# Kernel tuning notes

Hardware: AMD Instinct MI355X
Metric: run time of the kernel (lower is better)

## Reference

```python
import jax, jax.numpy as jnp
from jax import lax
import numpy as np

B, T = 32, 64
E = 64        # embed_dim
U = 32        # num_measurements
D0, D1 = 300, 100
S = 9         # speaker_num
CELL = 64     # output_cell_dim
C = 6         # n_classes
EPS = 1e-12


def setup_inputs() -> dict:
    key = jax.random.key(0)
    ks = jax.random.split(key, 16)
    sc = 1.0 / np.sqrt(E)
    n = lambda i, shape, s=1.0: (jax.random.normal(ks[i], shape, jnp.float32) * s)
    return {
        "x0": n(0, (B, T, D0)),
        "x1": n(1, (B, T, D1)),
        "smask": jax.random.uniform(ks[2], (B, T, S), jnp.float32),
        "umask": jnp.ones((B, T), jnp.float32),
        "W_ih0": n(3, (4 * E, D0), sc), "W_hh0": n(4, (4 * E, E), sc),
        "b_ih0": n(5, (4 * E,), sc), "b_hh0": n(6, (4 * E,), sc),
        "W_ih1": n(7, (4 * E, D1), sc), "W_hh1": n(8, (4 * E, E), sc),
        "b_ih1": n(9, (4 * E,), sc), "b_hh1": n(10, (4 * E,), sc),
        "phase_table": jax.random.uniform(ks[11], (S, E), jnp.float32, -np.pi, np.pi),
        "meas_kernel": jax.random.uniform(ks[12], (U, E, 2), jnp.float32),
        "W1": n(13, (CELL, 2 * U), 0.1), "b1": jnp.zeros((CELL,), jnp.float32),
        "W2": n(14, (C, CELL), 0.1), "b2": jnp.zeros((C,), jnp.float32),
    }


def _lstm_tanh(x, um, Wih, Whh, bih, bhh):
    # torch.nn.LSTMCell (gate order i,f,g,o) + extra tanh applied to h each step;
    # the tanh-ed h is carried as the recurrent state (dropout = identity in eval).
    b, t, _ = x.shape
    e = Whh.shape[1]

    def step(carry, inp):
        h, c = carry
        xt, ut = inp
        g = (xt * ut[:, None]) @ Wih.T + bih + h @ Whh.T + bhh
        i, f, gg, o = jnp.split(g, 4, axis=-1)
        c = jax.nn.sigmoid(f) * c + jax.nn.sigmoid(i) * jnp.tanh(gg)
        h = jnp.tanh(jax.nn.sigmoid(o) * jnp.tanh(c))
        return (h, c), h

    h0 = jnp.zeros((b, e), x.dtype)
    _, hs = lax.scan(step, (h0, h0), (jnp.swapaxes(x, 0, 1), um.T))
    return jnp.swapaxes(hs, 0, 1)  # (B,T,E)


def _measure(amp, phase, kernel):
    # pure state v = cos(phase)*amp + i sin(phase)*amp; rho = |v><v|
    r = jnp.cos(phase) * amp
    im = jnp.sin(phase) * amp
    rho_r = jnp.einsum('bti,btj->btij', r, r) + jnp.einsum('bti,btj->btij', im, im)
    rho_i = jnp.einsum('bti,btj->btij', im, r) - jnp.einsum('bti,btj->btij', r, im)
    u = kernel.shape[0]
    norm = jnp.clip(jnp.linalg.norm(kernel.reshape(u, -1), axis=-1), EPS)
    kn = kernel / norm[:, None, None]
    kr, ki = kn[..., 0], kn[..., 1]
    Pr = jnp.einsum('ui,uj->uij', kr, kr) + jnp.einsum('ui,uj->uij', ki, ki)
    Pi = jnp.einsum('ui,uj->uij', ki, kr) - jnp.einsum('ui,uj->uij', kr, ki)
    return jnp.einsum('btij,uij->btu', rho_r, Pr) - jnp.einsum('btij,uij->btu', rho_i, Pi)


def reference(x0, x1, smask, umask, W_ih0, W_hh0, b_ih0, b_hh0,
              W_ih1, W_hh1, b_ih1, b_hh1, phase_table, meas_kernel,
              W1, b1, W2, b2):
    h0 = _lstm_tanh(x0, umask, W_ih0, W_hh0, b_ih0, b_hh0)
    h1 = _lstm_tanh(x1, umask, W_ih1, W_hh1, b_ih1, b_hh1)
    norm = lambda h: h / jnp.clip(jnp.linalg.norm(h, axis=-1, keepdims=True), EPS)
    phase = phase_table[jnp.argmax(smask, axis=-1)]  # (B,T,E); table shared by both modalities
    m = jnp.concatenate([_measure(norm(h0), phase, meas_kernel),
                         _measure(norm(h1), phase, meas_kernel)], axis=-1)
    hid = jax.nn.relu(m @ W1.T + b1)
    pred = jnp.tanh(hid @ W2.T + b2)
    return jax.nn.log_softmax(pred, axis=2)
```

## Files before the change

kernel.cpp:

```cpp
#include <hip/hip_runtime.h>

typedef unsigned short ushort_t;
typedef unsigned int uint_t;
typedef float f32x2 __attribute__((ext_vector_type(2)));

__device__ __forceinline__ float bf2f(ushort_t v) {
  union { uint_t u; float f; } x; x.u = ((uint_t)v) << 16; return x.f;
}
__device__ __forceinline__ float lo16(uint_t u) {
  union { uint_t u; float f; } x; x.u = u << 16; return x.f;
}
__device__ __forceinline__ float hi16(uint_t u) {
  union { uint_t u; float f; } x; x.u = u & 0xffff0000u; return x.f;
}
__device__ __forceinline__ ushort_t f2bf(float f) {
  union { float f; uint_t u; } x; x.f = f;
  uint_t u = x.u;
  uint_t r = (u + 0x7fffu + ((u >> 16) & 1u)) >> 16;
  return (ushort_t)r;
}
__device__ __forceinline__ bool is_bf16(const void* um) {
  return *(const uint_t*)um == 0x3F803F80u;
}
__device__ __forceinline__ float ld_dual(const void* p, int i, bool isb) {
  return isb ? bf2f(((const ushort_t*)p)[i]) : ((const float*)p)[i];
}
__device__ __forceinline__ float frcp(float x) { return __builtin_amdgcn_rcpf(x); }
__device__ __forceinline__ float fsig(float x) { return frcp(1.f + __expf(-x)); }
__device__ __forceinline__ float ftanh(float x) {
  return fmaf(2.f, frcp(1.f + __expf(-2.f * x)), -1.f);
}

#if defined(__has_builtin)
#if __has_builtin(__builtin_elementwise_fma)
#define FMA2(a, b, c) __builtin_elementwise_fma((a), (b), (c))
#endif
#endif
#ifndef FMA2
__device__ __forceinline__ f32x2 fma2_fb(f32x2 a, f32x2 b, f32x2 c) {
  c.x = fmaf(a.x, b.x, c.x); c.y = fmaf(a.y, b.y, c.y); return c;
}
#define FMA2(a, b, c) fma2_fb((a), (b), (c))
#endif

__device__ __forceinline__ float dpp_add_xor1(float v) {
  const int r = __builtin_amdgcn_update_dpp(0, __float_as_int(v), 0xB1, 0xF, 0xF, true);
  return v + __int_as_float(r);
}
__device__ __forceinline__ float dpp_add_xor2(float v) {
  const int r = __builtin_amdgcn_update_dpp(0, __float_as_int(v), 0x4E, 0xF, 0xF, true);
  return v + __int_as_float(r);
}

#define PROJ_LDW 108

template <int D, bool ISB>
__device__ __forceinline__ void proj_body(
    const void* __restrict__ x, const void* __restrict__ um,
    const void* __restrict__ Wih, const void* __restrict__ bih,
    const void* __restrict__ bhh, float* __restrict__ xw,
    int rtile, int gtile, float* __restrict__ xs, float* __restrict__ ws)
{
  const int tid = threadIdx.x;
  const int r0 = rtile * 32;
  const int g0 = gtile * 32;
  const int rt = tid >> 4;
  const int gt = tid & 15;
  float a00 = 0.f, a01 = 0.f, a10 = 0.f, a11 = 0.f;

  for (int kt = 0; kt < D; kt += 100) {
    for (int i = tid; i < 800; i += 256) {
      const int r = i / 25;
      const int k4 = (i - r * 25) * 4;
      if (ISB) {
        const uint2 xv = *(const uint2*)((const ushort_t*)x + (r0 + r) * D + kt + k4);
        *(float4*)(xs + r * PROJ_LDW + k4) =
            make_float4(lo16(xv.x), hi16(xv.x), lo16(xv.y), hi16(xv.y));
        const uint2 wv = *(const uint2*)((const ushort_t*)Wih + (g0 + r) * D + kt + k4);
        *(float4*)(ws + r * PROJ_LDW + k4) =
            make_float4(lo16(wv.x), hi16(wv.x), lo16(wv.y), hi16(wv.y));
      } else {
        *(float4*)(xs + r * PROJ_LDW + k4) =
            *(const float4*)((const float*)x + (r0 + r) * D + kt + k4);
        *(float4*)(ws + r * PROJ_LDW + k4) =
            *(const float4*)((const float*)Wih + (g0 + r) * D + kt + k4);
      }
    }
    __syncthreads();
#pragma unroll 5
    for (int k = 0; k < 100; k += 4) {
      const float4 xa = *(const float4*)(xs + rt * PROJ_LDW + k);
      const float4 xb = *(const float4*)(xs + (rt + 16) * PROJ_LDW + k);
      const float4 wa = *(const float4*)(ws + gt * PROJ_LDW + k);
      const float4 wb = *(const float4*)(ws + (gt + 16) * PROJ_LDW + k);
      a00 = fmaf(xa.x, wa.x, a00); a00 = fmaf(xa.y, wa.y, a00);
      a00 = fmaf(xa.z, wa.z, a00); a00 = fmaf(xa.w, wa.w, a00);
      a01 = fmaf(xa.x, wb.x, a01); a01 = fmaf(xa.y, wb.y, a01);
      a01 = fmaf(xa.z, wb.z, a01); a01 = fmaf(xa.w, wb.w, a01);
      a10 = fmaf(xb.x, wa.x, a10); a10 = fmaf(xb.y, wa.y, a10);
      a10 = fmaf(xb.z, wa.z, a10); a10 = fmaf(xb.w, wa.w, a10);
      a11 = fmaf(xb.x, wb.x, a11); a11 = fmaf(xb.y, wb.y, a11);
      a11 = fmaf(xb.z, wb.z, a11); a11 = fmaf(xb.w, wb.w, a11);
    }
    __syncthreads();
  }

  const int ra = r0 + rt, rb = ra + 16;
  const int ga = g0 + gt, gb = ga + 16;
  const float ba = ld_dual(bih, ga, ISB) + ld_dual(bhh, ga, ISB);
  const float bb = ld_dual(bih, gb, ISB) + ld_dual(bhh, gb, ISB);
  const float ua = ld_dual(um, ra, ISB);
  const float ub = ld_dual(um, rb, ISB);
  const int pa = ((ga & 63) << 2) | (ga >> 6);
  const int pb = ((gb & 63) << 2) | (gb >> 6);
  xw[ra * 256 + pa] = fmaf(a00, ua, ba);
  xw[ra * 256 + pb] = fmaf(a01, ua, bb);
  xw[rb * 256 + pa] = fmaf(a10, ub, ba);
  xw[rb * 256 + pb] = fmaf(a11, ub, bb);
}

__global__ __launch_bounds__(256) void proj_both(
    const void* __restrict__ x0, const void* __restrict__ x1,
    const void* __restrict__ um,
    const void* __restrict__ Wih0, const void* __restrict__ bih0,
    const void* __restrict__ bhh0,
    const void* __restrict__ Wih1, const void* __restrict__ bih1,
    const void* __restrict__ bhh1,
    float* __restrict__ xw0, float* __restrict__ xw1)
{
  __shared__ __align__(16) float xs[32 * PROJ_LDW];
  __shared__ __align__(16) float ws[32 * PROJ_LDW];
  const bool isb = is_bf16(um);
  const int bid = blockIdx.x;
  const int l = bid >> 9;
  const int t = bid & 511;
  const int rtile = t >> 3;
  const int gtile = t & 7;
  if (l == 0) {
    if (isb) proj_body<300, true>(x0, um, Wih0, bih0, bhh0, xw0, rtile, gtile, xs, ws);
    else     proj_body<300, false>(x0, um, Wih0, bih0, bhh0, xw0, rtile, gtile, xs, ws);
  } else {
    if (isb) proj_body<100, true>(x1, um, Wih1, bih1, bhh1, xw1, rtile, gtile, xs, ws);
    else     proj_body<100, false>(x1, um, Wih1, bih1, bhh1, xw1, rtile, gtile, xs, ws);
  }
}

__global__ __launch_bounds__(256, 1) void lstm_k(
    const float* __restrict__ xw0, const float* __restrict__ xw1,
    const void* __restrict__ Whh0, const void* __restrict__ Whh1,
    const void* __restrict__ um,
    float* __restrict__ h0r, float* __restrict__ h1r)
{
  __shared__ __align__(16) float xws[64 * 256];
  __shared__ __align__(16) float hist[65 * 64];

  const int bid = blockIdx.x;
  const int l = bid >> 5;
  const int b = bid & 31;
  const float* xw = (l ? xw1 : xw0) + b * 64 * 256;
  const void* Whh = (l ? Whh1 : Whh0);
  float* hr = (l ? h1r : h0r) + b * 64 * 64;
  const int tid = threadIdx.x;
  const int e = tid >> 2;
  const int q = tid & 3;
  const int k0 = q << 4;
  const bool isb = is_bf16(um);

  for (int i = tid; i < 4096; i += 256)
    *(float4*)(xws + i * 4) = *(const float4*)(xw + i * 4);
  if (tid < 64) hist[tid] = 0.f;

  f32x2 w2[4][8];
  if (isb) {
#pragma unroll
    for (int t = 0; t < 4; ++t) {
      const ushort_t* wr = (const ushort_t*)Whh + (t * 64 + e) * 64 + k0;
#pragma unroll
      for (int j = 0; j < 16; j += 8) {
        const uint4 v = *(const uint4*)(wr + j);
        w2[t][(j >> 1) + 0] = f32x2{lo16(v.x), hi16(v.x)};
        w2[t][(j >> 1) + 1] = f32x2{lo16(v.y), hi16(v.y)};
        w2[t][(j >> 1) + 2] = f32x2{lo16(v.z), hi16(v.z)};
        w2[t][(j >> 1) + 3] = f32x2{lo16(v.w), hi16(v.w)};
      }
    }
  } else {
#pragma unroll
    for (int t = 0; t < 4; ++t) {
      const float* wr = (const float*)Whh + (t * 64 + e) * 64 + k0;
#pragma unroll
      for (int j = 0; j < 16; j += 4) {
        const float4 v = *(const float4*)(wr + j);
        w2[t][(j >> 1) + 0] = f32x2{v.x, v.y};
        w2[t][(j >> 1) + 1] = f32x2{v.z, v.w};
      }
    }
  }
  __syncthreads();

  float c = 0.f;
  float gin = xws[tid];
  for (int s = 0; s < 64; ++s) {
    const float* hp = hist + s * 64 + k0;
    f32x2 P0 = {q == 0 ? gin : 0.f, 0.f};
    f32x2 P1 = {q == 1 ? gin : 0.f, 0.f};
    f32x2 P2 = {q == 2 ? gin : 0.f, 0.f};
    f32x2 P3 = {q == 3 ? gin : 0.f, 0.f};
#pragma unroll
    for (int j = 0; j < 16; j += 4) {
      const float4 hv = *(const float4*)(hp + j);
      const f32x2 hA = {hv.x, hv.y}, hB = {hv.z, hv.w};
      const int jp = j >> 1;
      P0 = FMA2(w2[0][jp], hA, P0); P0 = FMA2(w2[0][jp + 1], hB, P0);
      P1 = FMA2(w2[1][jp], hA, P1); P1 = FMA2(w2[1][jp + 1], hB, P1);
      P2 = FMA2(w2[2][jp], hA, P2); P2 = FMA2(w2[2][jp + 1], hB, P2);
      P3 = FMA2(w2[3][jp], hA, P3); P3 = FMA2(w2[3][jp + 1], hB, P3);
    }
    float p0 = P0.x + P0.y;
    float p1 = P1.x + P1.y;
    float p2 = P2.x + P2.y;
    float p3 = P3.x + P3.y;
    p0 = dpp_add_xor1(p0); p0 = dpp_add_xor2(p0);
    p1 = dpp_add_xor1(p1); p1 = dpp_add_xor2(p1);
    p2 = dpp_add_xor1(p2); p2 = dpp_add_xor2(p2);
    p3 = dpp_add_xor1(p3); p3 = dpp_add_xor2(p3);
    const float yi = fsig(p0);
    const float yf = fsig(p1);
    const float yg = ftanh(p2);
    const float yo = fsig(p3);
    c = fmaf(yf, c, yi * yg);
    const float h = ftanh(yo * ftanh(c));
    if (q == 0) hist[(s + 1) * 64 + e] = h;
    if (s + 1 < 64) gin = xws[(s + 1) * 256 + tid];
    __syncthreads();
  }
  for (int i = tid; i < 1024; i += 256)
    *(float4*)(hr + i * 4) = *(const float4*)(hist + 64 + i * 4);
}

__global__ __launch_bounds__(256) void head_k(
    const float* __restrict__ h0r, const float* __restrict__ h1r,
    const void* __restrict__ smask, const void* __restrict__ um,
    const void* __restrict__ ptab, const void* __restrict__ mker,
    const void* __restrict__ W1, const void* __restrict__ b1,
    const void* __restrict__ W2, const void* __restrict__ b2,
    void* __restrict__ out)
{
  __shared__ float2 knT[64][32];
  __shared__ float w1T[64][65];
  __shared__ float w2T[64][9];
  __shared__ float b1s[64];
  __shared__ float b2s[8];
  __shared__ float rim[4][4][64];
  __shared__ float msh[4][64];
  __shared__ float hidsh[4][64];
  __shared__ float psh[4][8];

  const int tid = threadIdx.x;
  const bool isb = is_bf16(um);
  {
    const int u = tid >> 3, sub = tid & 7;
    float vr[8], vi[8];
    float ssq = 0.f;
#pragma unroll
    for (int qq = 0; qq < 8; ++qq) {
      const int e = sub * 8 + qq;
      if (isb) {
        const uint_t kk = ((const uint_t*)mker)[u * 64 + e];
        vr[qq] = lo16(kk); vi[qq] = hi16(kk);
      } else {
        const float2 kk = ((const float2*)mker)[u * 64 + e];
        vr[qq] = kk.x; vi[qq] = kk.y;
      }
      ssq = fmaf(vr[qq], vr[qq], ssq);
      ssq = fmaf(vi[qq], vi[qq], ssq);
    }
    ssq += __shfl_xor(ssq, 1);
    ssq += __shfl_xor(ssq, 2);
    ssq += __shfl_xor(ssq, 4);
    const float rn = 1.f / fmaxf(sqrtf(ssq), 1e-12f);
#pragma unroll
    for (int qq = 0; qq < 8; ++qq) {
      const int e = sub * 8 + qq;
      knT[e][u] = make_float2(vr[qq] * rn, vi[qq] * rn);
    }
  }
  for (int i = tid; i < 4096; i += 256) {
    const int j = i >> 6, ll = i & 63;
    w1T[ll][j] = ld_dual(W1, i, isb);
  }
  if (tid < 64) b1s[tid] = ld_dual(b1, tid, isb);
  for (int i = tid; i < 384; i += 256) {
    const int cc = i >> 6, j = i & 63;
    w2T[j][cc] = ld_dual(W2, i, isb);
  }
  if (tid < 6) b2s[tid] = ld_dual(b2, tid, isb);
  __syncthreads();

  const int wv = tid >> 6, lane = tid & 63;
  const int item = blockIdx.x * 4 + wv;
  const float h0raw = h0r[item * 64 + lane];
  const float h1raw = h1r[item * 64 + lane];
  float ss0 = h0raw * h0raw, ss1 = h1raw * h1raw;
#pragma unroll
  for (int m = 1; m < 64; m <<= 1) {
    ss0 += __shfl_xor(ss0, m);
    ss1 += __shfl_xor(ss1, m);
  }
  const float h0 = h0raw / fmaxf(sqrtf(ss0), 1e-12f);
  const float h1 = h1raw / fmaxf(sqrtf(ss1), 1e-12f);

  int idx = 0;
  if (lane == 0) {
    float best = -1e30f;
#pragma unroll
    for (int si = 0; si < 9; ++si) {
      const float v = ld_dual(smask, item * 9 + si, isb);
      if (v > best) { best = v; idx = si; }
    }
  }
  idx = __shfl(idx, 0, 64);
  const float ph = ld_dual(ptab, idx * 64 + lane, isb);
  float sr, cr;
  __sincosf(ph, &sr, &cr);
  rim[wv][0][lane] = cr * h0;
  rim[wv][1][lane] = sr * h0;
  rim[wv][2][lane] = cr * h1;
  rim[wv][3][lane] = sr * h1;
  __syncthreads();
  {
    const int u = lane & 31;
    const float* ra = rim[wv][(lane >= 32) ? 2 : 0];
    const float* ia = rim[wv][(lane >= 32) ? 3 : 1];
    float ar = 0.f, ai = 0.f;
#pragma unroll 8
    for (int e = 0; e < 64; ++e) {
      const float2 k = knT[e][u];
      const float rr = ra[e], ii = ia[e];
      ar = fmaf(rr, k.x, ar);
      ar = fmaf(-ii, k.y, ar);
      ai = fmaf(rr, k.y, ai);
      ai = fmaf(ii, k.x, ai);
    }
    msh[wv][lane] = fmaf(ar, ar, ai * ai);
  }
  __syncthreads();
  {
    float acc = b1s[lane];
#pragma unroll 8
    for (int L = 0; L < 64; ++L)
      acc = fmaf(msh[wv][L], w1T[L][lane], acc);
    hidsh[wv][lane] = fmaxf(acc, 0.f);
  }
  __syncthreads();
  if (lane < 6) {
    float a2 = b2s[lane];
#pragma unroll 8
    for (int j = 0; j < 64; ++j)
      a2 = fmaf(hidsh[wv][j], w2T[j][lane], a2);
    psh[wv][lane] = ftanh(a2);
  }
  __syncthreads();
  if (lane < 6) {
    const float p = psh[wv][lane];
    float mx = psh[wv][0];
#pragma unroll
    for (int cc = 1; cc < 6; ++cc) mx = fmaxf(mx, psh[wv][cc]);
    float sum = 0.f;
#pragma unroll
    for (int cc = 0; cc < 6; ++cc) sum += __expf(psh[wv][cc] - mx);
    const float res = p - mx - __logf(sum);
    if (isb) ((ushort_t*)out)[item * 6 + lane] = f2bf(res);
    else     ((float*)out)[item * 6 + lane] = res;
  }
}

extern "C" void kernel_launch(void* const* d_in, const int* in_sizes, int n_in,
                              void* d_out, int out_size, void* d_ws, size_t ws_size,
                              hipStream_t stream)
{
  (void)in_sizes; (void)n_in; (void)out_size; (void)ws_size;
  const void* x0    = d_in[0];
  const void* x1    = d_in[1];
  const void* smask = d_in[2];
  const void* um    = d_in[3];
  const void* Wih0  = d_in[4];
  const void* Whh0  = d_in[5];
  const void* bih0  = d_in[6];
  const void* bhh0  = d_in[7];
  const void* Wih1  = d_in[8];
  const void* Whh1  = d_in[9];
  const void* bih1  = d_in[10];
  const void* bhh1  = d_in[11];
  const void* ptab  = d_in[12];
  const void* mker  = d_in[13];
  const void* W1    = d_in[14];
  const void* b1    = d_in[15];
  const void* W2    = d_in[16];
  const void* b2    = d_in[17];

  float* xw0 = (float*)d_ws;
  float* xw1 = xw0 + 2048 * 256;
  float* h0r = xw1 + 2048 * 256;
  float* h1r = h0r + 2048 * 64;

  hipLaunchKernelGGL(proj_both, dim3(1024), dim3(256), 0, stream,
                     x0, x1, um, Wih0, bih0, bhh0, Wih1, bih1, bhh1,
                     xw0, xw1);
  hipLaunchKernelGGL(lstm_k, dim3(64), dim3(256), 0, stream,
                     xw0, xw1, Whh0, Whh1, um, h0r, h1r);
  hipLaunchKernelGGL(head_k, dim3(512), dim3(256), 0, stream,
                     h0r, h1r, smask, um, ptab, mker, W1, b1, W2, b2,
                     d_out);
}
```

Baseline: 148.4 us.

## Map each LSTM sequence to one wavefront to remove block barriers

Each batch sequence of the recurrent kernel now runs on a single 64-lane wavefront, with four sequences per block and 16 blocks in total. Each lane holds a full 64-wide row for all four gates in registers, so the DPP cross-lane reductions and the per-step __syncthreads disappear. The hidden state moves through a small per-wave LDS buffer. Input projections are prefetched from global memory one step ahead, and h is written straight to global memory each step. In exchange, each lane runs four times more serial FMAs per step, needs about 256 registers just for the weights, and the grid shrinks to 16 blocks.

```diff
diff --git a/kernel.cpp b/kernel.cpp
--- a/kernel.cpp
+++ b/kernel.cpp
@@ -42,15 +42,6 @@
 }
 #define FMA2(a, b, c) fma2_fb((a), (b), (c))
 #endif
-
-__device__ __forceinline__ float dpp_add_xor1(float v) {
-  const int r = __builtin_amdgcn_update_dpp(0, __float_as_int(v), 0xB1, 0xF, 0xF, true);
-  return v + __int_as_float(r);
-}
-__device__ __forceinline__ float dpp_add_xor2(float v) {
-  const int r = __builtin_amdgcn_update_dpp(0, __float_as_int(v), 0x4E, 0xF, 0xF, true);
-  return v + __int_as_float(r);
-}
 
 #define PROJ_LDW 108
 
@@ -151,64 +142,57 @@
     const void* __restrict__ um,
     float* __restrict__ h0r, float* __restrict__ h1r)
 {
-  __shared__ __align__(16) float xws[64 * 256];
-  __shared__ __align__(16) float hist[65 * 64];
-
+  __shared__ __align__(16) float wstage[256 * 68];
+  __shared__ __align__(16) float hsh[4][64];
+
+  const int tid = threadIdx.x;
+  const int wv = tid >> 6, lane = tid & 63;
   const int bid = blockIdx.x;
-  const int l = bid >> 5;
-  const int b = bid & 31;
+  const int l = bid >> 3;
+  const int b = (bid & 7) * 4 + wv;
   const float* xw = (l ? xw1 : xw0) + b * 64 * 256;
   const void* Whh = (l ? Whh1 : Whh0);
   float* hr = (l ? h1r : h0r) + b * 64 * 64;
-  const int tid = threadIdx.x;
-  const int e = tid >> 2;
-  const int q = tid & 3;
-  const int k0 = q << 4;
   const bool isb = is_bf16(um);
 
-  for (int i = tid; i < 4096; i += 256)
-    *(float4*)(xws + i * 4) = *(const float4*)(xw + i * 4);
-  if (tid < 64) hist[tid] = 0.f;
-
-  f32x2 w2[4][8];
-  if (isb) {
-#pragma unroll
-    for (int t = 0; t < 4; ++t) {
-      const ushort_t* wr = (const ushort_t*)Whh + (t * 64 + e) * 64 + k0;
-#pragma unroll
-      for (int j = 0; j < 16; j += 8) {
-        const uint4 v = *(const uint4*)(wr + j);
-        w2[t][(j >> 1) + 0] = f32x2{lo16(v.x), hi16(v.x)};
-        w2[t][(j >> 1) + 1] = f32x2{lo16(v.y), hi16(v.y)};
-        w2[t][(j >> 1) + 2] = f32x2{lo16(v.z), hi16(v.z)};
-        w2[t][(j >> 1) + 3] = f32x2{lo16(v.w), hi16(v.w)};
-      }
-    }
-  } else {
-#pragma unroll
-    for (int t = 0; t < 4; ++t) {
-      const float* wr = (const float*)Whh + (t * 64 + e) * 64 + k0;
-#pragma unroll
-      for (int j = 0; j < 16; j += 4) {
-        const float4 v = *(const float4*)(wr + j);
-        w2[t][(j >> 1) + 0] = f32x2{v.x, v.y};
-        w2[t][(j >> 1) + 1] = f32x2{v.z, v.w};
-      }
-    }
-  }
-  __syncthreads();
+  for (int i = tid; i < 4096; i += 256) {
+    const int row = i >> 4, k4 = (i & 15) << 2;
+    float4 v;
+    if (isb) {
+      const uint2 wu = *(const uint2*)((const ushort_t*)Whh + row * 64 + k4);
+      v = make_float4(lo16(wu.x), hi16(wu.x), lo16(wu.y), hi16(wu.y));
+    } else {
+      v = *(const float4*)((const float*)Whh + row * 64 + k4);
+    }
+    *(float4*)(wstage + row * 68 + k4) = v;
+  }
+  hsh[wv][lane] = 0.f;
+  __syncthreads();
+
+  f32x2 w2[4][32];
+#pragma unroll
+  for (int t = 0; t < 4; ++t) {
+    const float* wr = wstage + (t * 64 + lane) * 68;
+#pragma unroll
+    for (int j = 0; j < 64; j += 4) {
+      const float4 v = *(const float4*)(wr + j);
+      w2[t][(j >> 1) + 0] = f32x2{v.x, v.y};
+      w2[t][(j >> 1) + 1] = f32x2{v.z, v.w};
+    }
+  }
 
   float c = 0.f;
-  float gin = xws[tid];
+  float4 gin4 = *(const float4*)(xw + lane * 4);
+#pragma unroll 1
   for (int s = 0; s < 64; ++s) {
-    const float* hp = hist + s * 64 + k0;
-    f32x2 P0 = {q == 0 ? gin : 0.f, 0.f};
-    f32x2 P1 = {q == 1 ? gin : 0.f, 0.f};
-    f32x2 P2 = {q == 2 ? gin : 0.f, 0.f};
-    f32x2 P3 = {q == 3 ? gin : 0.f, 0.f};
-#pragma unroll
-    for (int j = 0; j < 16; j += 4) {
-      const float4 hv = *(const float4*)(hp + j);
+    const float4 ginN = *(const float4*)(xw + ((s + 1) & 63) * 256 + lane * 4);
+    f32x2 P0 = {gin4.x, 0.f};
+    f32x2 P1 = {gin4.y, 0.f};
+    f32x2 P2 = {gin4.z, 0.f};
+    f32x2 P3 = {gin4.w, 0.f};
+#pragma unroll
+    for (int j = 0; j < 64; j += 4) {
+      const float4 hv = *(const float4*)(&hsh[wv][j]);
       const f32x2 hA = {hv.x, hv.y}, hB = {hv.z, hv.w};
       const int jp = j >> 1;
       P0 = FMA2(w2[0][jp], hA, P0); P0 = FMA2(w2[0][jp + 1], hB, P0);
@@ -216,26 +200,22 @@
       P2 = FMA2(w2[2][jp], hA, P2); P2 = FMA2(w2[2][jp + 1], hB, P2);
       P3 = FMA2(w2[3][jp], hA, P3); P3 = FMA2(w2[3][jp + 1], hB, P3);
     }
-    float p0 = P0.x + P0.y;
-    float p1 = P1.x + P1.y;
-    float p2 = P2.x + P2.y;
-    float p3 = P3.x + P3.y;
-    p0 = dpp_add_xor1(p0); p0 = dpp_add_xor2(p0);
-    p1 = dpp_add_xor1(p1); p1 = dpp_add_xor2(p1);
-    p2 = dpp_add_xor1(p2); p2 = dpp_add_xor2(p2);
-    p3 = dpp_add_xor1(p3); p3 = dpp_add_xor2(p3);
+    const float p0 = P0.x + P0.y;
+    const float p1 = P1.x + P1.y;
+    const float p2 = P2.x + P2.y;
+    const float p3 = P3.x + P3.y;
     const float yi = fsig(p0);
     const float yf = fsig(p1);
     const float yg = ftanh(p2);
     const float yo = fsig(p3);
     c = fmaf(yf, c, yi * yg);
     const float h = ftanh(yo * ftanh(c));
-    if (q == 0) hist[(s + 1) * 64 + e] = h;
-    if (s + 1 < 64) gin = xws[(s + 1) * 256 + tid];
-    __syncthreads();
-  }
-  for (int i = tid; i < 1024; i += 256)
-    *(float4*)(hr + i * 4) = *(const float4*)(hist + 64 + i * 4);
+    hr[s * 64 + lane] = h;
+    hsh[wv][lane] = h;
+    asm volatile("s_waitcnt lgkmcnt(0)" ::: "memory");
+    __builtin_amdgcn_sched_barrier(0);
+    gin4 = ginN;
+  }
 }
 
 __global__ __launch_bounds__(256) void head_k(
@@ -407,7 +387,7 @@
   hipLaunchKernelGGL(proj_both, dim3(1024), dim3(256), 0, stream,
                      x0, x1, um, Wih0, bih0, bhh0, Wih1, bih1, bhh1,
                      xw0, xw1);
-  hipLaunchKernelGGL(lstm_k, dim3(64), dim3(256), 0, stream,
+  hipLaunchKernelGGL(lstm_k, dim3(16), dim3(256), 0, stream,
                      xw0, xw1, Whh0, Whh1, um, h0r, h1r);
   hipLaunchKernelGGL(head_k, dim3(512), dim3(256), 0, stream,
                      h0r, h1r, smask, um, ptab, mker, W1, b1, W2, b2,
```

Result: slower. 190.8 us (+28.6%).
